# Kernel optimization log

Hardware: AMD Instinct MI355X
Metric: run time of the kernel (lower is better)

The kernel has to match this reference:

```python
import jax, jax.numpy as jnp
import numpy as np

WIN = 7
SHIFT = 3
HEADS = 6
EPS = 1e-5


def _rel_pos_index(ws):
    coords = np.stack(np.meshgrid(np.arange(ws), np.arange(ws), indexing='ij')).reshape(2, -1)
    rel = (coords[:, :, None] - coords[:, None, :]).transpose(1, 2, 0)  # (N, N, 2)
    rel[..., 0] += ws - 1
    rel[..., 1] += ws - 1
    rel[..., 0] *= 2 * ws - 1
    return jnp.asarray(rel.sum(-1).reshape(-1))  # (N*N,)


def _attn_mask(H, W, ws, ss):
    img = np.zeros((H, W))
    sl = (slice(0, -ws), slice(-ws, -ss), slice(-ss, None))
    cnt = 0
    for hs in sl:
        for wss in sl:
            img[hs, wss] = cnt
            cnt += 1
    mw = img.reshape(H // ws, ws, W // ws, ws).transpose(0, 2, 1, 3).reshape(-1, ws * ws)
    am = mw[:, None, :] - mw[:, :, None]  # (nw, N, N): mw[j]-mw[i]
    return jnp.asarray(np.where(am != 0, -1e9, 0.0).astype(np.float32))


def _layernorm(x, g, b):
    mu = x.mean(-1, keepdims=True)
    var = ((x - mu) ** 2).mean(-1, keepdims=True)
    return (x - mu) * jax.lax.rsqrt(var + EPS) * g + b


def setup_inputs() -> dict:
    key = jax.random.key(0)
    ks = jax.random.split(key, 6)
    B, H, W, C = 4, 224, 224, 192
    return {
        'x': jax.random.normal(ks[0], (B, H * W, C), jnp.float32),
        'norm1_g': jnp.ones((C,), jnp.float32),
        'norm1_b': jnp.zeros((C,), jnp.float32),
        'qkv_w': jax.random.normal(ks[1], (C, 3 * C), jnp.float32) * 0.02,
        'qkv_b': jnp.zeros((3 * C,), jnp.float32),
        'rpb_table': jax.random.normal(ks[2], ((2 * WIN - 1) ** 2, HEADS), jnp.float32) * 0.02,
        'proj_w': jax.random.normal(ks[3], (C, C), jnp.float32) * 0.02,
        'proj_b': jnp.zeros((C,), jnp.float32),
        'norm2_g': jnp.ones((C,), jnp.float32),
        'norm2_b': jnp.zeros((C,), jnp.float32),
        'fc1_w': jax.random.normal(ks[4], (C, 4 * C), jnp.float32) * 0.02,
        'fc1_b': jnp.zeros((4 * C,), jnp.float32),
        'fc2_w': jax.random.normal(ks[5], (4 * C, C), jnp.float32) * 0.02,
        'fc2_b': jnp.zeros((C,), jnp.float32),
        'h': 224,
        'w': 224,
    }


def reference(x, norm1_g, norm1_b, qkv_w, qkv_b, rpb_table, proj_w, proj_b,
              norm2_g, norm2_b, fc1_w, fc1_b, fc2_w, fc2_b, h, w):
    B, L, C = x.shape
    ch = C // HEADS
    N = WIN * WIN
    nh, nw = h // WIN, w // WIN
    rel_idx = _rel_pos_index(WIN)
    mask = _attn_mask(h, w, WIN, SHIFT)  # (nh*nw, N, N)

    shortcut = x
    xn = _layernorm(x, norm1_g, norm1_b).reshape(B, h, w, C)
    xs = jnp.roll(xn, (-SHIFT, -SHIFT), axis=(1, 2))
    # window partition -> (B*nh*nw, N, C)
    xw = xs.reshape(B, nh, WIN, nw, WIN, C).transpose(0, 1, 3, 2, 4, 5).reshape(B * nh * nw, N, C)

    qkv = (xw @ qkv_w + qkv_b).reshape(-1, N, 3, HEADS, ch).transpose(2, 0, 3, 1, 4)
    q, k, v = qkv[0], qkv[1], qkv[2]  # (NW, HEADS, N, ch)
    scale = ch ** -0.5
    attn = jnp.einsum('whic,whjc->whij', q * scale, k)
    bias = rpb_table[rel_idx].reshape(N, N, HEADS).transpose(2, 0, 1)  # (HEADS, N, N)
    attn = attn + bias[None]
    attn = attn.reshape(B, nh * nw, HEADS, N, N) + mask[None, :, None]
    attn = jax.nn.softmax(attn, axis=-1).reshape(B * nh * nw, HEADS, N, N)

    out = jnp.einsum('whij,whjc->whic', attn, v).transpose(0, 2, 1, 3).reshape(-1, N, C)
    out = out @ proj_w + proj_b
    # window reverse + roll back
    out = out.reshape(B, nh, nw, WIN, WIN, C).transpose(0, 1, 3, 2, 4, 5).reshape(B, h, w, C)
    out = jnp.roll(out, (SHIFT, SHIFT), axis=(1, 2)).reshape(B, L, C)

    x = shortcut + out
    xn2 = _layernorm(x, norm2_g, norm2_b)
    hid = jax.nn.gelu(xn2 @ fc1_w + fc1_b, approximate=False)
    return x + (hid @ fc2_w + fc2_b)
```

## Files before the change

kernel.cpp:

```cpp
#include <hip/hip_runtime.h>
#include <stdint.h>

#define MB    50176
#define CDIM  192

typedef __attribute__((ext_vector_type(8))) short bf16x8;
typedef __attribute__((ext_vector_type(4))) float f32x4;

#define WFENCE do{ asm volatile("s_waitcnt lgkmcnt(0)" ::: "memory"); \
                   __builtin_amdgcn_sched_barrier(0); }while(0)

__device__ __forceinline__ float wsum(float v){
  #pragma unroll
  for (int m=32;m>=1;m>>=1) v += __shfl_xor(v,m,64);
  return v;
}
__device__ __forceinline__ float bfbits2f(uint32_t h){
  union{uint32_t u; float f;} x; x.u = h<<16; return x.f;
}
__device__ __forceinline__ uint16_t f2bfbits(float f){
  union{float ff; uint32_t u;} x; x.ff = f;
  return (uint16_t)((x.u + 0x7FFFu + ((x.u>>16)&1u)) >> 16);
}
__device__ __forceinline__ void gload16(const void* g, void* l){
  __builtin_amdgcn_global_load_lds(
      (const __attribute__((address_space(1))) uint32_t*)g,
      (__attribute__((address_space(3))) uint32_t*)l, 16, 0, 0);
}
__device__ __forceinline__ size_t row2tok(int r_g){
  int widx = r_g/49, tpos = r_g - widx*49;
  int b = widx>>10, rem = widx&1023;
  int h = (rem>>5)*7 + tpos/7 + 3; if (h>=224) h-=224;
  int w = (rem&31)*7 + (tpos - (tpos/7)*7) + 3; if (w>=224) w-=224;
  return (size_t)b*MB + (size_t)h*224 + w;
}

__global__ __launch_bounds__(256) void prep_kernel(
    const float* __restrict__ qkv_w, const float* __restrict__ proj_w,
    const float* __restrict__ fc1_w, const float* __restrict__ fc2_w,
    const float* __restrict__ rpb,
    uint16_t* __restrict__ qkvW, uint16_t* __restrict__ prjW,
    uint16_t* __restrict__ fc1W, uint16_t* __restrict__ fc2W,
    float* __restrict__ btbl){
  int idx = blockIdx.x*256 + threadIdx.x;
  if (idx < 110592){ int k=idx/576, n=idx-k*576; qkvW[n*192+k]=f2bfbits(qkv_w[idx]); return; }
  idx -= 110592;
  if (idx < 36864){ int k=idx/192, n=idx-k*192; prjW[n*192+k]=f2bfbits(proj_w[idx]); return; }
  idx -= 36864;
  if (idx < 147456){ int k=idx/768, n=idx-k*768; fc1W[n*192+k]=f2bfbits(fc1_w[idx]); return; }
  idx -= 147456;
  if (idx < 147456){ int k=idx/192, n=idx-k*192; fc2W[n*768+k]=f2bfbits(fc2_w[idx]); return; }
  idx -= 147456;
  if (idx >= 98304) return;
  int j = idx & 63, i = (idx>>6) & 63;
  int hd = (idx>>12) % 6, cls = (idx>>12)/6;
  float v = -1e9f;
  if (i < 49 && j < 49){
    int dh = i/7 - j/7, dw = i%7 - j%7;
    v = rpb[((dh+6)*13 + (dw+6))*6 + hd];
    int cH = cls>>1, cW = cls&1;
    int li = (cH ? (i/7 < 4 ? 1 : 2) : 0)*3 + (cW ? (i%7 < 4 ? 1 : 2) : 0);
    int lj = (cH ? (j/7 < 4 ? 1 : 2) : 0)*3 + (cW ? (j%7 < 4 ? 1 : 2) : 0);
    if (li != lj) v = -1e9f;
  }
  btbl[idx] = v;
}

__global__ __launch_bounds__(256) void ln1_kernel(
    const float* __restrict__ x, const float* __restrict__ g,
    const float* __restrict__ bt, uint16_t* __restrict__ dst, int row0){
  int wid_l = (int)((blockIdx.x*256u + threadIdx.x) >> 6);
  int lane  = threadIdx.x & 63;
  size_t sidx = row2tok(row0 + wid_l);
  const float* s = x + sidx*CDIM;
  float v0=s[lane], v1=s[lane+64], v2=s[lane+128];
  float mu  = wsum(v0+v1+v2) * (1.f/192.f);
  float var = wsum(v0*v0+v1*v1+v2*v2)*(1.f/192.f) - mu*mu;
  float rs  = rsqrtf(var + 1e-5f);
  uint16_t* d = dst + (size_t)wid_l*CDIM;
  d[lane]     = f2bfbits((v0-mu)*rs*g[lane]     + bt[lane]);
  d[lane+64]  = f2bfbits((v1-mu)*rs*g[lane+64]  + bt[lane+64]);
  d[lane+128] = f2bfbits((v2-mu)*rs*g[lane+128] + bt[lane+128]);
}

enum { EPI_QKV=0, EPI_FC1=2, EPI_FC2=3 };

template<int EPI, int K, int NN>
__global__ __launch_bounds__(256) void mgemm(
    const uint16_t* __restrict__ A, const uint16_t* __restrict__ WT,
    const float* __restrict__ bias, void* __restrict__ outp,
    const uint16_t* __restrict__ resid, int row0){
  __shared__ __attribute__((aligned(16))) char As[2][128*128];
  __shared__ __attribute__((aligned(16))) char Bs[2][64*128];
  __shared__ int tokt[128];
  const int tid  = threadIdx.x;
  const int lane = tid & 63;
  const int wid  = tid >> 6;
  const int brow = blockIdx.y * 128;
  const int bcol = blockIdx.x * 64;

  f32x4 acc[4][2];
  #pragma unroll
  for (int m=0;m<4;m++)
    #pragma unroll
    for (int n=0;n<2;n++) acc[m][n] = (f32x4){0.f,0.f,0.f,0.f};

  const int srow = lane >> 3;
  const int sg   = (lane & 7) ^ srow;
  const int wm = wid >> 1, wn = wid & 1;
  const int lrow16 = lane & 15, lkh = lane >> 4;

  if constexpr (EPI==EPI_FC2){
    if (tid < 128) tokt[tid] = (int)row2tok(row0 + brow + tid);
    asm volatile("s_waitcnt lgkmcnt(0)" ::: "memory");
  }

  #define STAGE(k0, Ad, Bd) do{ \
    _Pragma("unroll") \
    for (int c = 0; c < 4; c++){ \
      int ch = wid*4 + c; \
      gload16(A + (size_t)(brow + ch*8 + srow)*K + (k0) + sg*8, (Ad) + ch*1024); \
    } \
    _Pragma("unroll") \
    for (int c = 0; c < 2; c++){ \
      int ch = wid*2 + c; \
      gload16(WT + (size_t)(bcol + ch*8 + srow)*K + (k0) + sg*8, (Bd) + ch*1024); \
    } \
  }while(0)

  constexpr int NK = K/64;
  STAGE(0, As[0], Bs[0]);
  #pragma unroll
  for (int ki = 0; ki < NK; ki++){
    const int cur = ki & 1;
    if (ki+1 < NK){
      STAGE((ki+1)*64, As[cur^1], Bs[cur^1]);
      asm volatile("s_waitcnt vmcnt(6)" ::: "memory");
    } else {
      asm volatile("s_waitcnt vmcnt(0)" ::: "memory");
    }
    __builtin_amdgcn_s_barrier();
    __builtin_amdgcn_sched_barrier(0);

    bf16x8 af[4][2], bfr[2][2];
    #pragma unroll
    for (int m=0;m<4;m++)
      #pragma unroll
      for (int ks=0;ks<2;ks++){
        int arow = wm*64 + m*16 + lrow16;
        af[m][ks] = *(const bf16x8*)(As[cur] + arow*128 + (((ks*4+lkh) ^ (arow&7))<<4));
      }
    #pragma unroll
    for (int n=0;n<2;n++)
      #pragma unroll
      for (int ks=0;ks<2;ks++){
        int brn = wn*32 + n*16 + lrow16;
        bfr[n][ks] = *(const bf16x8*)(Bs[cur] + brn*128 + (((ks*4+lkh) ^ (brn&7))<<4));
      }
    #pragma unroll
    for (int m=0;m<4;m++)
      #pragma unroll
      for (int n=0;n<2;n++)
        #pragma unroll
        for (int ks=0;ks<2;ks++)
          acc[m][n] = __builtin_amdgcn_mfma_f32_16x16x32_bf16(
              af[m][ks], bfr[n][ks], acc[m][n], 0, 0, 0);
    if (ki+1 < NK) __builtin_amdgcn_s_barrier();
  }
  #undef STAGE

  float bi[2];
  #pragma unroll
  for (int n=0;n<2;n++) bi[n] = bias[bcol + wn*32 + n*16 + lrow16];
  #pragma unroll
  for (int m=0;m<4;m++){
    #pragma unroll
    for (int j=0;j<4;j++){
      int lr = wm*64 + m*16 + lkh*4 + j;
      int r  = brow + lr;
      if constexpr (EPI==EPI_QKV || EPI==EPI_FC1){
        #pragma unroll
        for (int n=0;n<2;n++){
          float v = acc[m][n][j] + bi[n];
          if constexpr (EPI==EPI_FC1)
            v = 0.5f*v*(1.f + erff(v*0.70710678118654752f));
          ((uint16_t*)outp)[(size_t)r*NN + bcol + wn*32 + n*16 + lrow16] = f2bfbits(v);
        }
      } else {
        size_t pr = (size_t)tokt[lr]*CDIM;
        #pragma unroll
        for (int n=0;n<2;n++){
          size_t p = pr + bcol + wn*32 + n*16 + lrow16;
          ((float*)outp)[p] = acc[m][n][j] + bi[n] + bfbits2f(resid[p]);
        }
      }
    }
  }
}

__global__ __launch_bounds__(384) void proj_ln2(
    const uint16_t* __restrict__ A, const uint16_t* __restrict__ WT,
    const float* __restrict__ pbias, const float* __restrict__ x,
    const float* __restrict__ g2, const float* __restrict__ b2,
    uint16_t* __restrict__ x2out, uint16_t* __restrict__ ln2out, int row0){
  __shared__ __attribute__((aligned(16))) char As[64*128];
  __shared__ __attribute__((aligned(16))) char Bs[192*128];
  __shared__ float stats[3][64][2];
  __shared__ int tokt[64];
  const int tid  = threadIdx.x;
  const int lane = tid & 63;
  const int wid  = tid >> 6;
  const int pm = wid / 3, pn = wid - pm*3;
  const int brow = blockIdx.x * 64;
  const int srow = lane >> 3;
  const int sg   = (lane & 7) ^ srow;
  const int r16 = lane & 15, t4 = lane >> 4;

  if (tid < 64) tokt[tid] = (int)row2tok(row0 + brow + tid);

  f32x4 acc[2][4];
  #pragma unroll
  for (int m=0;m<2;m++)
    #pragma unroll
    for (int n=0;n<4;n++) acc[m][n] = (f32x4){0.f,0.f,0.f,0.f};

  for (int k0 = 0; k0 < 192; k0 += 64){
    for (int ch = wid; ch < 8; ch += 6)
      gload16(A + (size_t)(brow + ch*8 + srow)*192 + k0 + sg*8, As + ch*1024);
    for (int ch = wid; ch < 24; ch += 6)
      gload16(WT + (size_t)(ch*8 + srow)*192 + k0 + sg*8, Bs + ch*1024);
    __syncthreads();

    bf16x8 af[2][2], bfr[4][2];
    #pragma unroll
    for (int m=0;m<2;m++)
      #pragma unroll
      for (int ks=0;ks<2;ks++){
        int arow = pm*32 + m*16 + r16;
        af[m][ks] = *(const bf16x8*)(As + arow*128 + (((ks*4+t4) ^ (arow&7))<<4));
      }
    #pragma unroll
    for (int n=0;n<4;n++)
      #pragma unroll
      for (int ks=0;ks<2;ks++){
        int brn = pn*64 + n*16 + r16;
        bfr[n][ks] = *(const bf16x8*)(Bs + brn*128 + (((ks*4+t4) ^ (brn&7))<<4));
      }
    #pragma unroll
    for (int m=0;m<2;m++)
      #pragma unroll
      for (int n=0;n<4;n++)
        #pragma unroll
        for (int ks=0;ks<2;ks++)
          acc[m][n] = __builtin_amdgcn_mfma_f32_16x16x32_bf16(
              af[m][ks], bfr[n][ks], acc[m][n], 0, 0, 0);
    __syncthreads();
  }

  float bi[4], g2v[4], b2v[4];
  #pragma unroll
  for (int n=0;n<4;n++){
    int c = pn*64 + n*16 + r16;
    bi[n] = pbias[c]; g2v[n] = g2[c]; b2v[n] = b2[c];
  }
  #pragma unroll
  for (int m=0;m<2;m++){
    #pragma unroll
    for (int j=0;j<4;j++){
      int lr = pm*32 + m*16 + t4*4 + j;
      size_t pr = (size_t)tokt[lr]*CDIM;
      float s1 = 0.f, s2 = 0.f;
      #pragma unroll
      for (int n=0;n<4;n++){
        int c = pn*64 + n*16 + r16;
        float y = acc[m][n][j] + bi[n] + x[pr + c];
        acc[m][n][j] = y;
        x2out[pr + c] = f2bfbits(y);
        s1 += y; s2 = fmaf(y, y, s2);
      }
      #pragma unroll
      for (int mk=1; mk<16; mk<<=1){
        s1 += __shfl_xor(s1, mk, 64);
        s2 += __shfl_xor(s2, mk, 64);
      }
      if (r16 == 0){ stats[pn][lr][0] = s1; stats[pn][lr][1] = s2; }
    }
  }
  __syncthreads();
  #pragma unroll
  for (int m=0;m<2;m++){
    #pragma unroll
    for (int j=0;j<4;j++){
      int lr = pm*32 + m*16 + t4*4 + j;
      float s1 = stats[0][lr][0] + stats[1][lr][0] + stats[2][lr][0];
      float s2 = stats[0][lr][1] + stats[1][lr][1] + stats[2][lr][1];
      float mu = s1*(1.f/192.f);
      float rs = rsqrtf(s2*(1.f/192.f) - mu*mu + 1e-5f);
      size_t wr = (size_t)(brow + lr)*CDIM;
      #pragma unroll
      for (int n=0;n<4;n++){
        int c = pn*64 + n*16 + r16;
        ln2out[wr + c] = f2bfbits((acc[m][n][j]-mu)*rs*g2v[n] + b2v[n]);
      }
    }
  }
}

__global__ __launch_bounds__(256) void attn_kernel(
    const uint16_t* __restrict__ qkv, const float* __restrict__ btbl,
    uint16_t* __restrict__ attnout, int win0){
  const int wv   = threadIdx.x >> 6;
  const int lane = threadIdx.x & 63;
  const int whd  = blockIdx.x*4 + wv;
  const int widx = whd/6, hd = whd - widx*6;
  const int r16 = lane & 15, t4 = lane >> 4;
  __shared__ uint16_t Vt[4][32][72];
  __shared__ uint16_t Pl[4][16][72];

  #pragma unroll
  for (int e=lane; e<32*16; e+=64){ Vt[wv][e>>4][48 + (e&15)] = 0; }
  for (int ch = lane; ch < 196; ch += 64){
    int j = ch >> 2, c0 = (ch&3)*8;
    const uint16_t* src = qkv + ((size_t)widx*49 + j)*576 + hd*32 + 384 + c0;
    uint4 v = *(const uint4*)src;
    uint32_t u[4] = {v.x, v.y, v.z, v.w};
    #pragma unroll
    for (int q=0;q<8;q++) Vt[wv][c0+q][j] = (uint16_t)(u[q>>1] >> ((q&1)*16));
  }

  bf16x8 kf[4];
  #pragma unroll
  for (int jt=0;jt<4;jt++)
    kf[jt] = *(const bf16x8*)(qkv + ((size_t)widx*49 + jt*16 + r16)*576 + hd*32 + 192 + t4*8);

  const int gw = win0 + widx;
  const int cls = ((((gw&1023)>>5)==31)<<1) | ((gw&31)==31);
  const float* tb = btbl + ((size_t)(cls*6 + hd) << 12);
  const float scale = 0.17677669529663689f;

  WFENCE;
  bf16x8 bv[2][2];
  #pragma unroll
  for (int ct=0;ct<2;ct++)
    #pragma unroll
    for (int ks=0;ks<2;ks++)
      bv[ct][ks] = *(const bf16x8*)&Vt[wv][ct*16 + r16][ks*32 + t4*8];

  #pragma unroll 2
  for (int it=0; it<4; it++){
    bf16x8 qf = *(const bf16x8*)(qkv + ((size_t)widx*49 + it*16 + r16)*576 + hd*32 + t4*8);
    f32x4 acc[4];
    #pragma unroll
    for (int jt=0;jt<4;jt++){
      acc[jt] = (f32x4){0.f,0.f,0.f,0.f};
      acc[jt] = __builtin_amdgcn_mfma_f32_16x16x32_bf16(kf[jt], qf, acc[jt], 0,0,0);
    }
    int i = it*16 + r16;
    float s[4][4];
    float m = -3.4e38f;
    #pragma unroll
    for (int jt=0;jt<4;jt++){
      float4 bvv = *(const float4*)(tb + i*64 + jt*16 + t4*4);
      float bb[4] = {bvv.x, bvv.y, bvv.z, bvv.w};
      #pragma unroll
      for (int r=0;r<4;r++){
        s[jt][r] = acc[jt][r]*scale + bb[r];
        m = fmaxf(m, s[jt][r]);
      }
    }
    m = fmaxf(m, __shfl_xor(m, 16, 64));
    m = fmaxf(m, __shfl_xor(m, 32, 64));
    float sum = 0.f;
    #pragma unroll
    for (int jt=0;jt<4;jt++)
      #pragma unroll
      for (int r=0;r<4;r++){
        s[jt][r] = __expf(s[jt][r] - m);
        sum += s[jt][r];
      }
    sum += __shfl_xor(sum, 16, 64);
    sum += __shfl_xor(sum, 32, 64);
    float inv = 1.f / sum;
    #pragma unroll
    for (int jt=0;jt<4;jt++){
      uint32_t lo = (uint32_t)f2bfbits(s[jt][0]*inv) | ((uint32_t)f2bfbits(s[jt][1]*inv) << 16);
      uint32_t hi = (uint32_t)f2bfbits(s[jt][2]*inv) | ((uint32_t)f2bfbits(s[jt][3]*inv) << 16);
      *(uint2*)&Pl[wv][r16][jt*16 + t4*4] = make_uint2(lo, hi);
    }
    asm volatile("s_waitcnt lgkmcnt(0)" ::: "memory");

    f32x4 o[2];
    o[0] = (f32x4){0.f,0.f,0.f,0.f};
    o[1] = (f32x4){0.f,0.f,0.f,0.f};
    #pragma unroll
    for (int ks=0;ks<2;ks++){
      bf16x8 pa = *(const bf16x8*)&Pl[wv][r16][ks*32 + t4*8];
      #pragma unroll
      for (int ct=0;ct<2;ct++)
        o[ct] = __builtin_amdgcn_mfma_f32_16x16x32_bf16(pa, bv[ct][ks], o[ct], 0,0,0);
    }
    #pragma unroll
    for (int r=0;r<4;r++){
      int i2 = it*16 + t4*4 + r;
      if (i2 < 49){
        size_t base = ((size_t)widx*49 + i2)*CDIM + hd*32;
        attnout[base + r16]      = f2bfbits(o[0][r]);
        attnout[base + 16 + r16] = f2bfbits(o[1][r]);
      }
    }
  }
}

extern "C" void kernel_launch(void* const* d_in, const int* in_sizes, int n_in,
                              void* d_out, int out_size, void* d_ws, size_t ws_size,
                              hipStream_t stream) {
  const float* x       = (const float*)d_in[0];
  const float* n1g     = (const float*)d_in[1];
  const float* n1b     = (const float*)d_in[2];
  const float* qkv_w   = (const float*)d_in[3];
  const float* qkv_b   = (const float*)d_in[4];
  const float* rpb     = (const float*)d_in[5];
  const float* proj_w  = (const float*)d_in[6];
  const float* proj_b  = (const float*)d_in[7];
  const float* n2g     = (const float*)d_in[8];
  const float* n2b     = (const float*)d_in[9];
  const float* fc1_w   = (const float*)d_in[10];
  const float* fc1_b   = (const float*)d_in[11];
  const float* fc2_w   = (const float*)d_in[12];
  const float* fc2_b   = (const float*)d_in[13];
  float* out = (float*)d_out;

  const int T = 200704;
  const size_t TBL = 221184 + 73728 + 294912 + 294912 + 393216;
  const size_t ABYTES  = (size_t)T*CDIM*2;
  size_t bq_bytes = (size_t)(T/2)*768*2;
  size_t need_full = ABYTES + bq_bytes + ABYTES + TBL;
  bool full = ws_size >= need_full;

  char* ws = (char*)d_ws;
  if (full){
    uint16_t* Abuf = (uint16_t*)ws;
    uint16_t* Bq   = (uint16_t*)(ws + ABYTES);
    uint16_t* X2   = (uint16_t*)(ws + ABYTES + bq_bytes);
    char* wbase    = ws + ABYTES + bq_bytes + ABYTES;
    uint16_t* qkvW = (uint16_t*)wbase;
    uint16_t* prjW = (uint16_t*)(wbase + 221184);
    uint16_t* fc1W = (uint16_t*)(wbase + 221184 + 73728);
    uint16_t* fc2W = (uint16_t*)(wbase + 221184 + 73728 + 294912);
    float*    btbl = (float*)(wbase + 221184 + 73728 + 294912 + 294912);

    prep_kernel<<<2112, 256, 0, stream>>>(qkv_w, proj_w, fc1_w, fc2_w, rpb,
                                          qkvW, prjW, fc1W, fc2W, btbl);
    const int H = T/2;
    ln1_kernel<<<T/4, 256, 0, stream>>>(x, n1g, n1b, Abuf, 0);
    for (int h=0; h<2; h++){
      uint16_t* Ah = Abuf + (size_t)h*H*CDIM;
      mgemm<EPI_QKV, 192, 576>
          <<<dim3(9, H/128), 256, 0, stream>>>(Ah, qkvW, qkv_b, (void*)Bq, nullptr, 0);
      attn_kernel<<<(H/49)*6/4, 256, 0, stream>>>(Bq, btbl, Ah, h*(H/49));
    }
    proj_ln2<<<T/64, 384, 0, stream>>>(Abuf, prjW, proj_b, x, n2g, n2b,
                                       X2, Abuf, 0);
    for (int h=0; h<2; h++){
      uint16_t* Ah = Abuf + (size_t)h*H*CDIM;
      mgemm<EPI_FC1, 192, 768>
          <<<dim3(12, H/128), 256, 0, stream>>>(Ah, fc1W, fc1_b, (void*)Bq, nullptr, 0);
      mgemm<EPI_FC2, 768, 192>
          <<<dim3(3, H/128), 256, 0, stream>>>(Bq, fc2W, fc2_b, (void*)out, X2, h*H);
    }
  } else {
    const int TC = MB, NW = TC/49;
    uint16_t* Abuf = (uint16_t*)ws;
    uint16_t* Bq   = (uint16_t*)(ws + (size_t)TC*CDIM*2);
    uint16_t* X2   = (uint16_t*)(ws + (size_t)TC*CDIM*2 + (size_t)TC*768*2);
    char* wbase    = ws + (size_t)TC*CDIM*2 + (size_t)TC*768*2 + ABYTES;
    uint16_t* qkvW = (uint16_t*)wbase;
    uint16_t* prjW = (uint16_t*)(wbase + 221184);
    uint16_t* fc1W = (uint16_t*)(wbase + 221184 + 73728);
    uint16_t* fc2W = (uint16_t*)(wbase + 221184 + 73728 + 294912);
    float*    btbl = (float*)(wbase + 221184 + 73728 + 294912 + 294912);

    prep_kernel<<<2112, 256, 0, stream>>>(qkv_w, proj_w, fc1_w, fc2_w, rpb,
                                          qkvW, prjW, fc1W, fc2W, btbl);
    for (int c = 0; c < 4; c++){
      int row0 = c*TC, win0 = row0/49;
      ln1_kernel<<<TC/4, 256, 0, stream>>>(x, n1g, n1b, Abuf, row0);
      mgemm<EPI_QKV, 192, 576>
          <<<dim3(9, TC/128), 256, 0, stream>>>(Abuf, qkvW, qkv_b, (void*)Bq, nullptr, 0);
      attn_kernel<<<NW*6/4, 256, 0, stream>>>(Bq, btbl, Abuf, win0);
      proj_ln2<<<TC/64, 384, 0, stream>>>(Abuf, prjW, proj_b, x, n2g, n2b,
                                          X2, Abuf, row0);
      mgemm<EPI_FC1, 192, 768>
          <<<dim3(12, TC/128), 256, 0, stream>>>(Abuf, fc1W, fc1_b, (void*)Bq, nullptr, 0);
      mgemm<EPI_FC2, 768, 192>
          <<<dim3(3, TC/128), 256, 0, stream>>>(Bq, fc2W, fc2_b, (void*)out, X2, row0);
    }
  }
}
```

Measured before the change: 756.7 us.

## Use tanh-form GELU, bf16 residual copy, and quarter-size chunked scratch

Replaces the erf-based GELU in the FC1 epilogue with a sigmoid/tanh approximation built on exp and a hardware reciprocal. LN1 also writes a bf16 copy of x, which proj_ln2 reads for the residual instead of the fp32 x, halving that traffic. The full-workspace path is split into four chunks instead of two so the FC1 scratch buffer is smaller and more likely to stay in cache, at the cost of more launches. The GELU approximation and the bf16 residual both add numerical error.

```diff
diff --git a/kernel.cpp b/kernel.cpp
--- a/kernel.cpp
+++ b/kernel.cpp
@@ -26,6 +26,10 @@
   __builtin_amdgcn_global_load_lds(
       (const __attribute__((address_space(1))) uint32_t*)g,
       (__attribute__((address_space(3))) uint32_t*)l, 16, 0, 0);
+}
+__device__ __forceinline__ float fast_gelu(float v){
+  float z = v*(1.5957691f + 0.07135481f*v*v);
+  return v * __builtin_amdgcn_rcpf(1.f + __expf(-z));
 }
 __device__ __forceinline__ size_t row2tok(int r_g){
   int widx = r_g/49, tpos = r_g - widx*49;
@@ -68,12 +72,19 @@
 
 __global__ __launch_bounds__(256) void ln1_kernel(
     const float* __restrict__ x, const float* __restrict__ g,
-    const float* __restrict__ bt, uint16_t* __restrict__ dst, int row0){
+    const float* __restrict__ bt, uint16_t* __restrict__ dst,
+    uint16_t* __restrict__ xbf, int row0){
   int wid_l = (int)((blockIdx.x*256u + threadIdx.x) >> 6);
   int lane  = threadIdx.x & 63;
   size_t sidx = row2tok(row0 + wid_l);
   const float* s = x + sidx*CDIM;
   float v0=s[lane], v1=s[lane+64], v2=s[lane+128];
+  if (xbf){
+    uint16_t* xb = xbf + sidx*CDIM;
+    xb[lane]     = f2bfbits(v0);
+    xb[lane+64]  = f2bfbits(v1);
+    xb[lane+128] = f2bfbits(v2);
+  }
   float mu  = wsum(v0+v1+v2) * (1.f/192.f);
   float var = wsum(v0*v0+v1*v1+v2*v2)*(1.f/192.f) - mu*mu;
   float rs  = rsqrtf(var + 1e-5f);
@@ -183,7 +194,7 @@
         for (int n=0;n<2;n++){
           float v = acc[m][n][j] + bi[n];
           if constexpr (EPI==EPI_FC1)
-            v = 0.5f*v*(1.f + erff(v*0.70710678118654752f));
+            v = fast_gelu(v);
           ((uint16_t*)outp)[(size_t)r*NN + bcol + wn*32 + n*16 + lrow16] = f2bfbits(v);
         }
       } else {
@@ -198,9 +209,11 @@
   }
 }
 
+template<bool XBF>
 __global__ __launch_bounds__(384) void proj_ln2(
     const uint16_t* __restrict__ A, const uint16_t* __restrict__ WT,
     const float* __restrict__ pbias, const float* __restrict__ x,
+    const uint16_t* __restrict__ xbf,
     const float* __restrict__ g2, const float* __restrict__ b2,
     uint16_t* __restrict__ x2out, uint16_t* __restrict__ ln2out, int row0){
   __shared__ __attribute__((aligned(16))) char As[64*128];
@@ -273,7 +286,8 @@
       #pragma unroll
       for (int n=0;n<4;n++){
         int c = pn*64 + n*16 + r16;
-        float y = acc[m][n][j] + bi[n] + x[pr + c];
+        float rv = XBF ? bfbits2f(xbf[pr + c]) : x[pr + c];
+        float y = acc[m][n][j] + bi[n] + rv;
         acc[m][n][j] = y;
         x2out[pr + c] = f2bfbits(y);
         s1 += y; s2 = fmaf(y, y, s2);
@@ -432,9 +446,9 @@
 
   const int T = 200704;
   const size_t TBL = 221184 + 73728 + 294912 + 294912 + 393216;
-  const size_t ABYTES  = (size_t)T*CDIM*2;
-  size_t bq_bytes = (size_t)(T/2)*768*2;
-  size_t need_full = ABYTES + bq_bytes + ABYTES + TBL;
+  const size_t ABYTES = (size_t)T*CDIM*2;
+  size_t bq_bytes = (size_t)(T/4)*768*2;
+  size_t need_full = ABYTES*3 + bq_bytes + TBL;
   bool full = ws_size >= need_full;
 
   char* ws = (char*)d_ws;
@@ -442,7 +456,8 @@
     uint16_t* Abuf = (uint16_t*)ws;
     uint16_t* Bq   = (uint16_t*)(ws + ABYTES);
     uint16_t* X2   = (uint16_t*)(ws + ABYTES + bq_bytes);
-    char* wbase    = ws + ABYTES + bq_bytes + ABYTES;
+    uint16_t* Xbf  = (uint16_t*)(ws + ABYTES*2 + bq_bytes);
+    char* wbase    = ws + ABYTES*3 + bq_bytes;
     uint16_t* qkvW = (uint16_t*)wbase;
     uint16_t* prjW = (uint16_t*)(wbase + 221184);
     uint16_t* fc1W = (uint16_t*)(wbase + 221184 + 73728);
@@ -451,22 +466,22 @@
 
     prep_kernel<<<2112, 256, 0, stream>>>(qkv_w, proj_w, fc1_w, fc2_w, rpb,
                                           qkvW, prjW, fc1W, fc2W, btbl);
-    const int H = T/2;
-    ln1_kernel<<<T/4, 256, 0, stream>>>(x, n1g, n1b, Abuf, 0);
-    for (int h=0; h<2; h++){
-      uint16_t* Ah = Abuf + (size_t)h*H*CDIM;
+    const int Q = T/4;
+    ln1_kernel<<<T/4, 256, 0, stream>>>(x, n1g, n1b, Abuf, Xbf, 0);
+    for (int h=0; h<4; h++){
+      uint16_t* Ah = Abuf + (size_t)h*Q*CDIM;
       mgemm<EPI_QKV, 192, 576>
-          <<<dim3(9, H/128), 256, 0, stream>>>(Ah, qkvW, qkv_b, (void*)Bq, nullptr, 0);
-      attn_kernel<<<(H/49)*6/4, 256, 0, stream>>>(Bq, btbl, Ah, h*(H/49));
-    }
-    proj_ln2<<<T/64, 384, 0, stream>>>(Abuf, prjW, proj_b, x, n2g, n2b,
-                                       X2, Abuf, 0);
-    for (int h=0; h<2; h++){
-      uint16_t* Ah = Abuf + (size_t)h*H*CDIM;
+          <<<dim3(9, Q/128), 256, 0, stream>>>(Ah, qkvW, qkv_b, (void*)Bq, nullptr, 0);
+      attn_kernel<<<(Q/49)*6/4, 256, 0, stream>>>(Bq, btbl, Ah, h*(Q/49));
+    }
+    proj_ln2<true><<<T/64, 384, 0, stream>>>(Abuf, prjW, proj_b, x, Xbf,
+                                             n2g, n2b, X2, Abuf, 0);
+    for (int h=0; h<4; h++){
+      uint16_t* Ah = Abuf + (size_t)h*Q*CDIM;
       mgemm<EPI_FC1, 192, 768>
-          <<<dim3(12, H/128), 256, 0, stream>>>(Ah, fc1W, fc1_b, (void*)Bq, nullptr, 0);
+          <<<dim3(12, Q/128), 256, 0, stream>>>(Ah, fc1W, fc1_b, (void*)Bq, nullptr, 0);
       mgemm<EPI_FC2, 768, 192>
-          <<<dim3(3, H/128), 256, 0, stream>>>(Bq, fc2W, fc2_b, (void*)out, X2, h*H);
+          <<<dim3(3, Q/128), 256, 0, stream>>>(Bq, fc2W, fc2_b, (void*)out, X2, h*Q);
     }
   } else {
     const int TC = MB, NW = TC/49;
@@ -484,12 +499,12 @@
                                           qkvW, prjW, fc1W, fc2W, btbl);
     for (int c = 0; c < 4; c++){
       int row0 = c*TC, win0 = row0/49;
-      ln1_kernel<<<TC/4, 256, 0, stream>>>(x, n1g, n1b, Abuf, row0);
+      ln1_kernel<<<TC/4, 256, 0, stream>>>(x, n1g, n1b, Abuf, nullptr, row0);
       mgemm<EPI_QKV, 192, 576>
           <<<dim3(9, TC/128), 256, 0, stream>>>(Abuf, qkvW, qkv_b, (void*)Bq, nullptr, 0);
       attn_kernel<<<NW*6/4, 256, 0, stream>>>(Bq, btbl, Abuf, win0);
-      proj_ln2<<<TC/64, 384, 0, stream>>>(Abuf, prjW, proj_b, x, n2g, n2b,
-                                          X2, Abuf, row0);
+      proj_ln2<false><<<TC/64, 384, 0, stream>>>(Abuf, prjW, proj_b, x, nullptr,
+                                                 n2g, n2b, X2, Abuf, row0);
       mgemm<EPI_FC1, 192, 768>
           <<<dim3(12, TC/128), 256, 0, stream>>>(Abuf, fc1W, fc1_b, (void*)Bq, nullptr, 0);
       mgemm<EPI_FC2, 768, 192>
```

Result: slower. 785.0 us (+3.7%).

## Make GEMM blocks loop over row tiles, use fast GELU, drop half-splitting

Applied to the files above, without the earlier changes.

The mgemm kernel now has each block handle GIT=4 consecutive 128-row tiles. The double-buffered prefetch runs continuously across tile boundaries, and the epilogue for one tile overlaps the loads for the next, which spreads per-block setup over more work. The FC1 epilogue swaps the exact erf GELU for a tanh-style sigmoid approximation built on __expf and a hardware reciprocal, trading some accuracy for cheaper math. In the full-workspace path, the two half-batch passes are merged into single launches by allocating the full-size intermediate buffer, which cuts launch count but uses more workspace memory.

```diff
diff --git a/kernel.cpp b/kernel.cpp
--- a/kernel.cpp
+++ b/kernel.cpp
@@ -26,6 +26,10 @@
   __builtin_amdgcn_global_load_lds(
       (const __attribute__((address_space(1))) uint32_t*)g,
       (__attribute__((address_space(3))) uint32_t*)l, 16, 0, 0);
+}
+__device__ __forceinline__ float fast_gelu(float v){
+  float z = v*(1.5957691f + 0.07135481f*v*v);
+  return v * __builtin_amdgcn_rcpf(1.f + __expf(-z));
 }
 __device__ __forceinline__ size_t row2tok(int r_g){
   int widx = r_g/49, tpos = r_g - widx*49;
@@ -84,6 +88,7 @@
 }
 
 enum { EPI_QKV=0, EPI_FC1=2, EPI_FC2=3 };
+#define GIT 4
 
 template<int EPI, int K, int NN>
 __global__ __launch_bounds__(256) void mgemm(
@@ -92,18 +97,12 @@
     const uint16_t* __restrict__ resid, int row0){
   __shared__ __attribute__((aligned(16))) char As[2][128*128];
   __shared__ __attribute__((aligned(16))) char Bs[2][64*128];
-  __shared__ int tokt[128];
+  __shared__ int tokt[GIT*128];
   const int tid  = threadIdx.x;
   const int lane = tid & 63;
   const int wid  = tid >> 6;
-  const int brow = blockIdx.y * 128;
-  const int bcol = blockIdx.x * 64;
-
-  f32x4 acc[4][2];
-  #pragma unroll
-  for (int m=0;m<4;m++)
-    #pragma unroll
-    for (int n=0;n<2;n++) acc[m][n] = (f32x4){0.f,0.f,0.f,0.f};
+  const int rbase = blockIdx.y * (GIT*128);
+  const int bcol  = blockIdx.x * 64;
 
   const int srow = lane >> 3;
   const int sg   = (lane & 7) ^ srow;
@@ -111,91 +110,106 @@
   const int lrow16 = lane & 15, lkh = lane >> 4;
 
   if constexpr (EPI==EPI_FC2){
-    if (tid < 128) tokt[tid] = (int)row2tok(row0 + brow + tid);
+    for (int e = tid; e < GIT*128; e += 256)
+      tokt[e] = (int)row2tok(row0 + rbase + e);
     asm volatile("s_waitcnt lgkmcnt(0)" ::: "memory");
   }
 
-  #define STAGE(k0, Ad, Bd) do{ \
+  float bi[2];
+  #pragma unroll
+  for (int n=0;n<2;n++) bi[n] = bias[bcol + wn*32 + n*16 + lrow16];
+
+  #define STAGE(brw, kk, Ad, Bd) do{ \
     _Pragma("unroll") \
     for (int c = 0; c < 4; c++){ \
       int ch = wid*4 + c; \
-      gload16(A + (size_t)(brow + ch*8 + srow)*K + (k0) + sg*8, (Ad) + ch*1024); \
+      gload16(A + (size_t)((brw) + ch*8 + srow)*K + (kk) + sg*8, (Ad) + ch*1024); \
     } \
     _Pragma("unroll") \
     for (int c = 0; c < 2; c++){ \
       int ch = wid*2 + c; \
-      gload16(WT + (size_t)(bcol + ch*8 + srow)*K + (k0) + sg*8, (Bd) + ch*1024); \
+      gload16(WT + (size_t)(bcol + ch*8 + srow)*K + (kk) + sg*8, (Bd) + ch*1024); \
     } \
   }while(0)
 
   constexpr int NK = K/64;
-  STAGE(0, As[0], Bs[0]);
-  #pragma unroll
-  for (int ki = 0; ki < NK; ki++){
-    const int cur = ki & 1;
-    if (ki+1 < NK){
-      STAGE((ki+1)*64, As[cur^1], Bs[cur^1]);
-      asm volatile("s_waitcnt vmcnt(6)" ::: "memory");
-    } else {
-      asm volatile("s_waitcnt vmcnt(0)" ::: "memory");
-    }
-    __builtin_amdgcn_s_barrier();
-    __builtin_amdgcn_sched_barrier(0);
-
-    bf16x8 af[4][2], bfr[2][2];
+  STAGE(rbase, 0, As[0], Bs[0]);
+  int s = 0;
+  #pragma unroll 1
+  for (int t = 0; t < GIT; t++){
+    const int brow = rbase + t*128;
+    f32x4 acc[4][2];
     #pragma unroll
     for (int m=0;m<4;m++)
       #pragma unroll
-      for (int ks=0;ks<2;ks++){
-        int arow = wm*64 + m*16 + lrow16;
-        af[m][ks] = *(const bf16x8*)(As[cur] + arow*128 + (((ks*4+lkh) ^ (arow&7))<<4));
-      }
-    #pragma unroll
-    for (int n=0;n<2;n++)
-      #pragma unroll
-      for (int ks=0;ks<2;ks++){
-        int brn = wn*32 + n*16 + lrow16;
-        bfr[n][ks] = *(const bf16x8*)(Bs[cur] + brn*128 + (((ks*4+lkh) ^ (brn&7))<<4));
-      }
-    #pragma unroll
-    for (int m=0;m<4;m++)
+      for (int n=0;n<2;n++) acc[m][n] = (f32x4){0.f,0.f,0.f,0.f};
+
+    #pragma unroll
+    for (int ki = 0; ki < NK; ki++, s++){
+      const int cur = s & 1;
+      if (s+1 < GIT*NK){
+        const int t2 = (ki+1==NK) ? t+1 : t;
+        const int k2 = (ki+1==NK) ? 0 : (ki+1)*64;
+        STAGE(rbase + t2*128, k2, As[cur^1], Bs[cur^1]);
+        asm volatile("s_waitcnt vmcnt(6)" ::: "memory");
+      } else {
+        asm volatile("s_waitcnt vmcnt(0)" ::: "memory");
+      }
+      __builtin_amdgcn_s_barrier();
+      __builtin_amdgcn_sched_barrier(0);
+
+      bf16x8 af[4][2], bfr[2][2];
+      #pragma unroll
+      for (int m=0;m<4;m++)
+        #pragma unroll
+        for (int ks=0;ks<2;ks++){
+          int arow = wm*64 + m*16 + lrow16;
+          af[m][ks] = *(const bf16x8*)(As[cur] + arow*128 + (((ks*4+lkh) ^ (arow&7))<<4));
+        }
       #pragma unroll
       for (int n=0;n<2;n++)
         #pragma unroll
-        for (int ks=0;ks<2;ks++)
-          acc[m][n] = __builtin_amdgcn_mfma_f32_16x16x32_bf16(
-              af[m][ks], bfr[n][ks], acc[m][n], 0, 0, 0);
-    if (ki+1 < NK) __builtin_amdgcn_s_barrier();
+        for (int ks=0;ks<2;ks++){
+          int brn = wn*32 + n*16 + lrow16;
+          bfr[n][ks] = *(const bf16x8*)(Bs[cur] + brn*128 + (((ks*4+lkh) ^ (brn&7))<<4));
+        }
+      #pragma unroll
+      for (int m=0;m<4;m++)
+        #pragma unroll
+        for (int n=0;n<2;n++)
+          #pragma unroll
+          for (int ks=0;ks<2;ks++)
+            acc[m][n] = __builtin_amdgcn_mfma_f32_16x16x32_bf16(
+                af[m][ks], bfr[n][ks], acc[m][n], 0, 0, 0);
+      if (s+1 < GIT*NK) __builtin_amdgcn_s_barrier();
+    }
+
+    #pragma unroll
+    for (int m=0;m<4;m++){
+      #pragma unroll
+      for (int j=0;j<4;j++){
+        int lr = wm*64 + m*16 + lkh*4 + j;
+        int r  = brow + lr;
+        if constexpr (EPI==EPI_QKV || EPI==EPI_FC1){
+          #pragma unroll
+          for (int n=0;n<2;n++){
+            float v = acc[m][n][j] + bi[n];
+            if constexpr (EPI==EPI_FC1)
+              v = fast_gelu(v);
+            ((uint16_t*)outp)[(size_t)r*NN + bcol + wn*32 + n*16 + lrow16] = f2bfbits(v);
+          }
+        } else {
+          size_t pr = (size_t)tokt[t*128 + lr]*CDIM;
+          #pragma unroll
+          for (int n=0;n<2;n++){
+            size_t p = pr + bcol + wn*32 + n*16 + lrow16;
+            ((float*)outp)[p] = acc[m][n][j] + bi[n] + bfbits2f(resid[p]);
+          }
+        }
+      }
+    }
   }
   #undef STAGE
-
-  float bi[2];
-  #pragma unroll
-  for (int n=0;n<2;n++) bi[n] = bias[bcol + wn*32 + n*16 + lrow16];
-  #pragma unroll
-  for (int m=0;m<4;m++){
-    #pragma unroll
-    for (int j=0;j<4;j++){
-      int lr = wm*64 + m*16 + lkh*4 + j;
-      int r  = brow + lr;
-      if constexpr (EPI==EPI_QKV || EPI==EPI_FC1){
-        #pragma unroll
-        for (int n=0;n<2;n++){
-          float v = acc[m][n][j] + bi[n];
-          if constexpr (EPI==EPI_FC1)
-            v = 0.5f*v*(1.f + erff(v*0.70710678118654752f));
-          ((uint16_t*)outp)[(size_t)r*NN + bcol + wn*32 + n*16 + lrow16] = f2bfbits(v);
-        }
-      } else {
-        size_t pr = (size_t)tokt[lr]*CDIM;
-        #pragma unroll
-        for (int n=0;n<2;n++){
-          size_t p = pr + bcol + wn*32 + n*16 + lrow16;
-          ((float*)outp)[p] = acc[m][n][j] + bi[n] + bfbits2f(resid[p]);
-        }
-      }
-    }
-  }
 }
 
 __global__ __launch_bounds__(384) void proj_ln2(
@@ -432,17 +446,17 @@
 
   const int T = 200704;
   const size_t TBL = 221184 + 73728 + 294912 + 294912 + 393216;
-  const size_t ABYTES  = (size_t)T*CDIM*2;
-  size_t bq_bytes = (size_t)(T/2)*768*2;
-  size_t need_full = ABYTES + bq_bytes + ABYTES + TBL;
+  const size_t ABYTES = (size_t)T*CDIM*2;
+  const size_t BQFULL = (size_t)T*768*2;
+  size_t need_full = ABYTES + BQFULL + ABYTES + TBL;
   bool full = ws_size >= need_full;
 
   char* ws = (char*)d_ws;
   if (full){
     uint16_t* Abuf = (uint16_t*)ws;
     uint16_t* Bq   = (uint16_t*)(ws + ABYTES);
-    uint16_t* X2   = (uint16_t*)(ws + ABYTES + bq_bytes);
-    char* wbase    = ws + ABYTES + bq_bytes + ABYTES;
+    uint16_t* X2   = (uint16_t*)(ws + ABYTES + BQFULL);
+    char* wbase    = ws + ABYTES + BQFULL + ABYTES;
     uint16_t* qkvW = (uint16_t*)wbase;
     uint16_t* prjW = (uint16_t*)(wbase + 221184);
     uint16_t* fc1W = (uint16_t*)(wbase + 221184 + 73728);
@@ -451,23 +465,16 @@
 
     prep_kernel<<<2112, 256, 0, stream>>>(qkv_w, proj_w, fc1_w, fc2_w, rpb,
                                           qkvW, prjW, fc1W, fc2W, btbl);
-    const int H = T/2;
     ln1_kernel<<<T/4, 256, 0, stream>>>(x, n1g, n1b, Abuf, 0);
-    for (int h=0; h<2; h++){
-      uint16_t* Ah = Abuf + (size_t)h*H*CDIM;
-      mgemm<EPI_QKV, 192, 576>
-          <<<dim3(9, H/128), 256, 0, stream>>>(Ah, qkvW, qkv_b, (void*)Bq, nullptr, 0);
-      attn_kernel<<<(H/49)*6/4, 256, 0, stream>>>(Bq, btbl, Ah, h*(H/49));
-    }
+    mgemm<EPI_QKV, 192, 576>
+        <<<dim3(9, T/(128*GIT)), 256, 0, stream>>>(Abuf, qkvW, qkv_b, (void*)Bq, nullptr, 0);
+    attn_kernel<<<(T/49)*6/4, 256, 0, stream>>>(Bq, btbl, Abuf, 0);
     proj_ln2<<<T/64, 384, 0, stream>>>(Abuf, prjW, proj_b, x, n2g, n2b,
                                        X2, Abuf, 0);
-    for (int h=0; h<2; h++){
-      uint16_t* Ah = Abuf + (size_t)h*H*CDIM;
-      mgemm<EPI_FC1, 192, 768>
-          <<<dim3(12, H/128), 256, 0, stream>>>(Ah, fc1W, fc1_b, (void*)Bq, nullptr, 0);
-      mgemm<EPI_FC2, 768, 192>
-          <<<dim3(3, H/128), 256, 0, stream>>>(Bq, fc2W, fc2_b, (void*)out, X2, h*H);
-    }
+    mgemm<EPI_FC1, 192, 768>
+        <<<dim3(12, T/(128*GIT)), 256, 0, stream>>>(Abuf, fc1W, fc1_b, (void*)Bq, nullptr, 0);
+    mgemm<EPI_FC2, 768, 192>
+        <<<dim3(3, T/(128*GIT)), 256, 0, stream>>>(Bq, fc2W, fc2_b, (void*)out, X2, 0);
   } else {
     const int TC = MB, NW = TC/49;
     uint16_t* Abuf = (uint16_t*)ws;
@@ -486,14 +493,14 @@
       int row0 = c*TC, win0 = row0/49;
       ln1_kernel<<<TC/4, 256, 0, stream>>>(x, n1g, n1b, Abuf, row0);
       mgemm<EPI_QKV, 192, 576>
-          <<<dim3(9, TC/128), 256, 0, stream>>>(Abuf, qkvW, qkv_b, (void*)Bq, nullptr, 0);
+          <<<dim3(9, TC/(128*GIT)), 256, 0, stream>>>(Abuf, qkvW, qkv_b, (void*)Bq, nullptr, 0);
       attn_kernel<<<NW*6/4, 256, 0, stream>>>(Bq, btbl, Abuf, win0);
       proj_ln2<<<TC/64, 384, 0, stream>>>(Abuf, prjW, proj_b, x, n2g, n2b,
                                           X2, Abuf, row0);
       mgemm<EPI_FC1, 192, 768>
-          <<<dim3(12, TC/128), 256, 0, stream>>>(Abuf, fc1W, fc1_b, (void*)Bq, nullptr, 0);
+          <<<dim3(12, TC/(128*GIT)), 256, 0, stream>>>(Abuf, fc1W, fc1_b, (void*)Bq, nullptr, 0);
       mgemm<EPI_FC2, 768, 192>
-          <<<dim3(3, TC/128), 256, 0, stream>>>(Bq, fc2W, fc2_b, (void*)out, X2, row0);
-    }
-  }
-}
+          <<<dim3(3, TC/(128*GIT)), 256, 0, stream>>>(Bq, fc2W, fc2_b, (void*)out, X2, row0);
+    }
+  }
+}
```

Measured after the change: 786.1 us. 1.04x slower.
